# Performance work log

Hardware: AMD Instinct MI355X
Metric: run time of the kernel (lower is better)

The kernel has to match this reference:

```python
import jax, jax.numpy as jnp
import numpy as np

TAU = 0.5      # init kwarg tau
LAMBD = 0.5    # init kwarg lambd
N, D, C = 4096, 1024, 512


def setup_inputs() -> dict:
    key = jax.random.key(0)
    k1, k2, k3 = jax.random.split(key, 3)
    return {
        "layer_embeds": jax.random.normal(k1, (N, D), dtype=jnp.float32),
        "y_true": jax.random.randint(k2, (N,), 0, C),
        "y_pred": jax.random.normal(k3, (N, C), dtype=jnp.float32),
    }


def _clce(x, y_true, y_pred):
    n = x.shape[0]
    # pairwise cosine similarity via one matmul (torch eps = 1e-8)
    norms = jnp.clip(jnp.linalg.norm(x, axis=1, keepdims=True), 1e-8)
    xn = x / norms
    sim = (xn @ xn.T + 1.0) * 0.5 * TAU          # [N, N]

    same = y_true[:, None] == y_true[None, :]    # diagonal is always True
    eye = jnp.eye(n, dtype=bool)
    pos_mask = same & ~eye                        # candidate positives (j != i)
    neg_mask = ~same                              # negatives (excludes diagonal)

    # slot 0: similarity to the FIRST positive j (in j order), else stays 0
    first_pos = jnp.argmax(pos_mask, axis=1)
    has_pos = pos_mask.any(axis=1)
    slot0 = jnp.where(has_pos,
                      jnp.take_along_axis(sim, first_pos[:, None], axis=1)[:, 0],
                      0.0)

    # negatives packed left-to-right into columns 1..; unfilled slots stay 0
    cum = jnp.cumsum(neg_mask, axis=1)            # 1-based slot per negative
    cols = jnp.where(neg_mask, cum, 2 * n - 1)    # non-negatives -> sink col
    rows = jnp.arange(n)[:, None]
    loss_temp = jnp.zeros((n, 2 * n), dtype=sim.dtype)
    loss_temp = loss_temp.at[rows, cols].add(jnp.where(neg_mask, sim, 0.0))
    loss_temp = loss_temp.at[:, 0].set(slot0)
    loss_temp = loss_temp[:, : 2 * n - 1]         # drop sink column -> [N, 2N-1]

    cl = -jax.nn.log_softmax(loss_temp, axis=1)[:, 0]
    cl = cl.sum() / n

    logp = jax.nn.log_softmax(y_pred, axis=1)
    ce = -jnp.take_along_axis(logp, y_true[:, None], axis=1).mean()

    return LAMBD * cl + (1.0 - LAMBD) * ce


def reference(layer_embeds, y_true, y_pred):
    return _clce(layer_embeds, y_true, y_pred)
```

## Files before the change

kernel.cpp:

```cpp
#include <hip/hip_runtime.h>
#include <hip/hip_bf16.h>

#define NR 4096
#define DIM 1024
#define NCLS 512

typedef __attribute__((ext_vector_type(4))) float f32x4;
typedef __attribute__((ext_vector_type(8))) int v8i;

static __device__ __forceinline__ unsigned int q4(float v) {
  unsigned int s = (v < 0.f) ? 8u : 0u;
  float a = fabsf(v);
  unsigned int c;
  if (a < 0.25f) c = 0;
  else if (a < 0.75f) c = 1;
  else if (a < 1.25f) c = 2;
  else if (a < 1.75f) c = 3;
  else if (a < 2.5f) c = 4;
  else if (a < 3.5f) c = 5;
  else if (a < 5.0f) c = 6;
  else c = 7;
  return s | c;
}

__global__ __launch_bounds__(256) void k_prep(const float* __restrict__ x,
                                              const int* __restrict__ y,
                                              const float* __restrict__ yp,
                                              unsigned char* __restrict__ xnp,
                                              int* __restrict__ cnt,
                                              int* __restrict__ fpos,
                                              float* __restrict__ slot0,
                                              float* __restrict__ ce,
                                              float* __restrict__ out) {
  const int b = blockIdx.x;
  const int tid = threadIdx.x;
  if (b < 1024) {
    int row = b * 4 + (tid >> 6);
    int lane = tid & 63;
    const float4* xr = reinterpret_cast<const float4*>(x + (size_t)row * DIM);
    float4 v[4];
    float s = 0.f;
#pragma unroll
    for (int it = 0; it < 4; ++it) {
      v[it] = xr[it * 64 + lane];
      s += v[it].x * v[it].x + v[it].y * v[it].y + v[it].z * v[it].z + v[it].w * v[it].w;
    }
#pragma unroll
    for (int d = 1; d < 64; d <<= 1) s += __shfl_xor(s, d);
    float inv = 32.0f / fmaxf(sqrtf(s), 1e-8f);
    unsigned char* xo = xnp + (size_t)row * 512;
#pragma unroll
    for (int it = 0; it < 4; ++it) {
      int k0 = (it * 64 + lane) * 4;
      int pos = (k0 >> 7) * 64 + ((k0 >> 5) & 3) * 16 + ((k0 & 31) >> 1);
      unsigned int n0 = q4(v[it].x * inv), n1 = q4(v[it].y * inv),
                   n2 = q4(v[it].z * inv), n3 = q4(v[it].w * inv);
      unsigned short pk =
          (unsigned short)(n0 | (n1 << 4) | (n2 << 8) | (n3 << 12));
      *(unsigned short*)(xo + pos) = pk;
    }
  } else if (b < 2048) {
    int row = (b - 1024) * 4 + (tid >> 6);
    int lane = tid & 63;
    const float4* p = reinterpret_cast<const float4*>(yp + (size_t)row * NCLS);
    float4 v0 = p[lane], v1 = p[lane + 64];
    float m = fmaxf(fmaxf(fmaxf(v0.x, v0.y), fmaxf(v0.z, v0.w)),
                    fmaxf(fmaxf(v1.x, v1.y), fmaxf(v1.z, v1.w)));
#pragma unroll
    for (int d = 1; d < 64; d <<= 1) m = fmaxf(m, __shfl_xor(m, d));
    float s = __expf(v0.x - m) + __expf(v0.y - m) + __expf(v0.z - m) + __expf(v0.w - m) +
              __expf(v1.x - m) + __expf(v1.y - m) + __expf(v1.z - m) + __expf(v1.w - m);
#pragma unroll
    for (int d = 1; d < 64; d <<= 1) s += __shfl_xor(s, d);
    if (lane == 0) {
      float py = yp[(size_t)row * NCLS + y[row]];
      ce[row] = logf(s) + m - py;
    }
  } else {
    __shared__ int ys[NR];
    __shared__ int scnt[NCLS], sm1[NCLS], sm2[NCLS];
    for (int j = tid; j < NR; j += 256) ys[j] = y[j];
    for (int c = tid; c < NCLS; c += 256) { scnt[c] = 0; sm1[c] = NR; sm2[c] = NR; }
    __syncthreads();
    for (int i = tid; i < NR; i += 256) {
      int c = ys[i];
      atomicAdd(&scnt[c], 1);
      atomicMin(&sm1[c], i);
    }
    __syncthreads();
    for (int i = tid; i < NR; i += 256) {
      int c = ys[i];
      if (sm1[c] != i) atomicMin(&sm2[c], i);
    }
    __syncthreads();
    for (int i = tid; i < NR; i += 256) {
      int c = ys[i];
      int m1 = sm1[c];
      int j = (m1 == i) ? ((sm2[c] >= NR) ? -1 : sm2[c]) : m1;
      fpos[i] = j;
      slot0[i] = 0.f;
    }
    for (int c = tid; c < NCLS; c += 256) cnt[c] = scnt[c];
    if (tid == 0) out[0] = 0.f;
  }
}


#define STAGE(SSLOT, GROWBASE, KT)                                               \
  {                                                                              \
    const char* _src = (const char*)xnp +                                        \
        (size_t)((GROWBASE) + srow) * 512 + (size_t)(KT) * 64 + scol;            \
    __builtin_amdgcn_global_load_lds(                                            \
        (const __attribute__((address_space(1))) void*)_src,                     \
        (__attribute__((address_space(3))) void*)(lds + (SSLOT) + tid * 16),     \
        16, 0, 0);                                                               \
  }

#define PHASE(BUFB, RP, LOADB, SSLOT, SBASE, SKT, VM)                            \
  {                                                                              \
    _Pragma("unroll") for (int mm = 0; mm < 2; ++mm) {                           \
      int4 t4 = *(const int4*)(lds + (BUFB) + ABaseW +                           \
                               ((RP) * 2 + mm) * 1024);                          \
      v8i tv = {t4.x, t4.y, t4.z, t4.w, 0, 0, 0, 0};                             \
      afr[mm] = tv;                                                              \
    }                                                                            \
    if (LOADB) {                                                                 \
      _Pragma("unroll") for (int nf = 0; nf < 2; ++nf) {                         \
        int4 t4 = *(const int4*)(lds + (BUFB) + BBaseW + nf * 1024);             \
        v8i tv = {t4.x, t4.y, t4.z, t4.w, 0, 0, 0, 0};                           \
        bfr[nf] = tv;                                                            \
      }                                                                          \
    }                                                                            \
    STAGE(SSLOT, SBASE, SKT)                                                     \
    if (VM) asm volatile("s_waitcnt vmcnt(1)" ::: "memory");                     \
    __builtin_amdgcn_s_barrier();                                                \
    asm volatile("s_waitcnt lgkmcnt(0)" ::: "memory");                           \
    __builtin_amdgcn_sched_barrier(0);                                           \
    __builtin_amdgcn_s_setprio(1);                                               \
    _Pragma("unroll") for (int mm = 0; mm < 2; ++mm)                             \
      _Pragma("unroll") for (int nf = 0; nf < 2; ++nf)                           \
        acc[(RP) * 2 + mm][nf] = __builtin_amdgcn_mfma_scale_f32_16x16x128_f8f6f4( \
            afr[mm], bfr[nf], acc[(RP) * 2 + mm][nf], 4, 4,                      \
            0, 0x7F7F7F7F, 0, 0x7F7F7F7F);                                       \
    __builtin_amdgcn_s_setprio(0);                                               \
    __builtin_amdgcn_sched_barrier(0);                                           \
    __builtin_amdgcn_s_barrier();                                                \
  }

__global__ __launch_bounds__(512, 2) void k_gemm(const unsigned char* __restrict__ xnp,
                                                 const int* __restrict__ y,
                                                 const int* __restrict__ fpos,
                                                 float* __restrict__ part,
                                                 float* __restrict__ slot0) {
  __shared__ char lds[32768];
  const int tid = threadIdx.x;
  const int w = tid >> 6, lane = tid & 63;
  const int wr = w >> 2, wcn = w & 3;
  const int r0 = lane & 15, klo = lane >> 4;

  const int bid = blockIdx.x;
  const int swzb = (bid & 7) * 128 + (bid >> 3);
  const int rb = swzb >> 5, cb = swzb & 31;
  const int rowbase = rb * 128, colbase = cb * 128;

  const int kread = (klo * 16) ^ ((r0 & 3) << 4);
  const int ABaseW = wr * 4096 + r0 * 64 + kread;
  const int BBaseW = 8192 + wcn * 2048 + r0 * 64 + kread;

  int srow, scol;
  {
    int D = tid * 16;
    int L = D ^ (((D >> 6) & 3) << 4);
    srow = L >> 6;
    scol = L & 63;
  }

  f32x4 acc[4][2] = {};

  STAGE(8192, colbase, 0)
  STAGE(0, rowbase, 0)
  STAGE(24576, colbase, 1)
  asm volatile("s_waitcnt vmcnt(1)" ::: "memory");
  __builtin_amdgcn_s_barrier();

  for (int i = 0; i < 4; ++i) {
    const int t1 = 2 * i + 1;
    const int tn = (2 * i + 2 < 8) ? 2 * i + 2 : 7;
    const int tn1 = (2 * i + 3 < 8) ? 2 * i + 3 : 7;
    v8i afr[2], bfr[2];
    PHASE(0,     0, 1, 16384, rowbase, t1, 0)
    PHASE(0,     1, 0, 8192,  colbase, tn, 1)
    PHASE(16384, 0, 1, 0,     rowbase, tn, 0)
    PHASE(16384, 1, 0, 24576, colbase, tn1, 1)
  }

  asm volatile("s_waitcnt vmcnt(0)" ::: "memory");
  __syncthreads();

  int* yrow_s = (int*)lds;
  int* ycol_s = (int*)(lds + 512);
  int* frow_s = (int*)(lds + 1024);
  float* rsum = (float*)(lds + 2048);
  if (tid < 128) {
    yrow_s[tid] = y[rowbase + tid];
    frow_s[tid] = fpos[rowbase + tid];
  } else if (tid < 256) {
    ycol_s[tid - 128] = y[colbase + tid - 128];
  }
  __syncthreads();

#pragma unroll
  for (int m = 0; m < 4; ++m) {
    float rs[4] = {0.f, 0.f, 0.f, 0.f};
    int rloc[4], yr[4], fr[4];
#pragma unroll
    for (int reg = 0; reg < 4; ++reg) {
      rloc[reg] = wr * 64 + m * 16 + klo * 4 + reg;
      yr[reg] = yrow_s[rloc[reg]];
      fr[reg] = frow_s[rloc[reg]];
    }
#pragma unroll
    for (int nf = 0; nf < 2; ++nf) {
      int cl = wcn * 32 + nf * 16 + r0;
      int yc = ycol_s[cl];
      int gc = colbase + cl;
#pragma unroll
      for (int reg = 0; reg < 4; ++reg) {
        float sv = acc[m][nf][reg] * (1.0f / 4096.f) + 0.25f;
        float e = (yr[reg] == yc) ? 0.f : __expf(sv);
        rs[reg] += e;
        if (fr[reg] == gc) slot0[rowbase + rloc[reg]] = sv;
      }
    }
#pragma unroll
    for (int d = 1; d < 16; d <<= 1)
#pragma unroll
      for (int reg = 0; reg < 4; ++reg) rs[reg] += __shfl_xor(rs[reg], d);
    if (r0 == 0) {
#pragma unroll
      for (int reg = 0; reg < 4; ++reg)
        rsum[rloc[reg] * 4 + wcn] = rs[reg];
    }
  }
  __syncthreads();
  if (tid < 128)
    part[(size_t)cb * NR + rowbase + tid] =
        rsum[tid * 4] + rsum[tid * 4 + 1] + rsum[tid * 4 + 2] + rsum[tid * 4 + 3];
}

__global__ __launch_bounds__(256) void k_final(const float* __restrict__ part,
                                               const float* __restrict__ slot0,
                                               const int* __restrict__ cnt,
                                               const int* __restrict__ y,
                                               const float* __restrict__ ce,
                                               float* __restrict__ out) {
  __shared__ float red[256];
  const int tid = threadIdx.x;
  const int r = blockIdx.x * 256 + tid;
  float S = 0.f;
#pragma unroll
  for (int b = 0; b < 32; ++b) S += part[(size_t)b * NR + r];
  float s0 = slot0[r];
  float zeros = 4094.0f + (float)cnt[y[r]];
  float cl = logf(__expf(s0) + S + zeros) - s0;
  red[tid] = 0.5f * (cl + ce[r]);
  __syncthreads();
  for (int s = 128; s > 0; s >>= 1) {
    if (tid < s) red[tid] += red[tid + s];
    __syncthreads();
  }
  if (tid == 0) atomicAdd(out, red[0] / (float)NR);
}

extern "C" void kernel_launch(void* const* d_in, const int* in_sizes, int n_in,
                              void* d_out, int out_size, void* d_ws, size_t ws_size,
                              hipStream_t stream) {
  const float* x = (const float*)d_in[0];
  const int* y = (const int*)d_in[1];
  const float* yp = (const float*)d_in[2];
  float* out = (float*)d_out;

  char* w = (char*)d_ws;
  unsigned char* xnp = (unsigned char*)w;
  int* cnt = (int*)(w + 2097152);
  int* fpos = (int*)(w + 2099200);
  float* slot0 = (float*)(w + 2115584);
  float* part = (float*)(w + 2131968);
  float* ce = (float*)(w + 2656256);

  k_prep<<<2049, 256, 0, stream>>>(x, y, yp, xnp, cnt, fpos, slot0, ce, out);
  k_gemm<<<1024, 512, 0, stream>>>(xnp, y, fpos, part, slot0);
  k_final<<<16, 256, 0, stream>>>(part, slot0, cnt, y, ce, out);
}
```

Measured before the change: 48.12 us.

## Enlarge GEMM tile to 256x128 with simple double-buffered K loop

The similarity GEMM tile grows from 128x128 to 256x128 per block, with the 8 waves rearranged as 4x2 and each wave holding a 64x64 accumulator (4x4 MFMA fragments). The launch goes from 1024 to 512 blocks. The hand-pipelined phase schedule with split barriers and priority changes is replaced by a plain double buffer: stage the next K chunk, compute the current one, then sync. This increases operand reuse per LDS load and halves the block count, at the cost of more LDS (48KB), more accumulator registers, fewer blocks to fill the CUs, and coarser load/compute overlap.

```diff
diff --git a/kernel.cpp b/kernel.cpp
--- a/kernel.cpp
+++ b/kernel.cpp
@@ -106,45 +106,24 @@
 }
 
 
-#define STAGE(SSLOT, GROWBASE, KT)                                               \
+#define STAGE_CHUNK(BUFB, KT)                                                    \
   {                                                                              \
-    const char* _src = (const char*)xnp +                                        \
-        (size_t)((GROWBASE) + srow) * 512 + (size_t)(KT) * 64 + scol;            \
+    _Pragma("unroll") for (int q = 0; q < 2; ++q) {                              \
+      const char* _srcA = (const char*)xnp +                                     \
+          (size_t)(rowbase + srowA[q]) * 512 + (size_t)(KT) * 64 + scolA[q];     \
+      __builtin_amdgcn_global_load_lds(                                          \
+          (const __attribute__((address_space(1))) void*)_srcA,                  \
+          (__attribute__((address_space(3))) void*)(lds + (BUFB) + q * 8192 +    \
+                                                    tid * 16),                   \
+          16, 0, 0);                                                             \
+    }                                                                            \
+    const char* _srcB = (const char*)xnp +                                       \
+        (size_t)(colbase + srowB) * 512 + (size_t)(KT) * 64 + scolB;             \
     __builtin_amdgcn_global_load_lds(                                            \
-        (const __attribute__((address_space(1))) void*)_src,                     \
-        (__attribute__((address_space(3))) void*)(lds + (SSLOT) + tid * 16),     \
+        (const __attribute__((address_space(1))) void*)_srcB,                    \
+        (__attribute__((address_space(3))) void*)(lds + (BUFB) + 16384 +         \
+                                                  tid * 16),                     \
         16, 0, 0);                                                               \
-  }
-
-#define PHASE(BUFB, RP, LOADB, SSLOT, SBASE, SKT, VM)                            \
-  {                                                                              \
-    _Pragma("unroll") for (int mm = 0; mm < 2; ++mm) {                           \
-      int4 t4 = *(const int4*)(lds + (BUFB) + ABaseW +                           \
-                               ((RP) * 2 + mm) * 1024);                          \
-      v8i tv = {t4.x, t4.y, t4.z, t4.w, 0, 0, 0, 0};                             \
-      afr[mm] = tv;                                                              \
-    }                                                                            \
-    if (LOADB) {                                                                 \
-      _Pragma("unroll") for (int nf = 0; nf < 2; ++nf) {                         \
-        int4 t4 = *(const int4*)(lds + (BUFB) + BBaseW + nf * 1024);             \
-        v8i tv = {t4.x, t4.y, t4.z, t4.w, 0, 0, 0, 0};                           \
-        bfr[nf] = tv;                                                            \
-      }                                                                          \
-    }                                                                            \
-    STAGE(SSLOT, SBASE, SKT)                                                     \
-    if (VM) asm volatile("s_waitcnt vmcnt(1)" ::: "memory");                     \
-    __builtin_amdgcn_s_barrier();                                                \
-    asm volatile("s_waitcnt lgkmcnt(0)" ::: "memory");                           \
-    __builtin_amdgcn_sched_barrier(0);                                           \
-    __builtin_amdgcn_s_setprio(1);                                               \
-    _Pragma("unroll") for (int mm = 0; mm < 2; ++mm)                             \
-      _Pragma("unroll") for (int nf = 0; nf < 2; ++nf)                           \
-        acc[(RP) * 2 + mm][nf] = __builtin_amdgcn_mfma_scale_f32_16x16x128_f8f6f4( \
-            afr[mm], bfr[nf], acc[(RP) * 2 + mm][nf], 4, 4,                      \
-            0, 0x7F7F7F7F, 0, 0x7F7F7F7F);                                       \
-    __builtin_amdgcn_s_setprio(0);                                               \
-    __builtin_amdgcn_sched_barrier(0);                                           \
-    __builtin_amdgcn_s_barrier();                                                \
   }
 
 __global__ __launch_bounds__(512, 2) void k_gemm(const unsigned char* __restrict__ xnp,
@@ -152,81 +131,103 @@
                                                  const int* __restrict__ fpos,
                                                  float* __restrict__ part,
                                                  float* __restrict__ slot0) {
-  __shared__ char lds[32768];
+  __shared__ char lds[49152];
   const int tid = threadIdx.x;
   const int w = tid >> 6, lane = tid & 63;
-  const int wr = w >> 2, wcn = w & 3;
+  const int wr = w >> 1, wc = w & 1;
   const int r0 = lane & 15, klo = lane >> 4;
 
   const int bid = blockIdx.x;
-  const int swzb = (bid & 7) * 128 + (bid >> 3);
+  const int swzb = (bid & 7) * 64 + (bid >> 3);
   const int rb = swzb >> 5, cb = swzb & 31;
-  const int rowbase = rb * 128, colbase = cb * 128;
+  const int rowbase = rb * 256, colbase = cb * 128;
 
   const int kread = (klo * 16) ^ ((r0 & 3) << 4);
-  const int ABaseW = wr * 4096 + r0 * 64 + kread;
-  const int BBaseW = 8192 + wcn * 2048 + r0 * 64 + kread;
-
-  int srow, scol;
+  const int ABase = wr * 4096 + r0 * 64 + kread;
+  const int BBase = 16384 + wc * 4096 + r0 * 64 + kread;
+
+  int srowA[2], scolA[2], srowB, scolB;
+#pragma unroll
+  for (int q = 0; q < 2; ++q) {
+    int D = q * 8192 + tid * 16;
+    int L = D ^ (((D >> 6) & 3) << 4);
+    srowA[q] = L >> 6;
+    scolA[q] = L & 63;
+  }
   {
     int D = tid * 16;
     int L = D ^ (((D >> 6) & 3) << 4);
-    srow = L >> 6;
-    scol = L & 63;
-  }
-
-  f32x4 acc[4][2] = {};
-
-  STAGE(8192, colbase, 0)
-  STAGE(0, rowbase, 0)
-  STAGE(24576, colbase, 1)
-  asm volatile("s_waitcnt vmcnt(1)" ::: "memory");
-  __builtin_amdgcn_s_barrier();
-
-  for (int i = 0; i < 4; ++i) {
-    const int t1 = 2 * i + 1;
-    const int tn = (2 * i + 2 < 8) ? 2 * i + 2 : 7;
-    const int tn1 = (2 * i + 3 < 8) ? 2 * i + 3 : 7;
-    v8i afr[2], bfr[2];
-    PHASE(0,     0, 1, 16384, rowbase, t1, 0)
-    PHASE(0,     1, 0, 8192,  colbase, tn, 1)
-    PHASE(16384, 0, 1, 0,     rowbase, tn, 0)
-    PHASE(16384, 1, 0, 24576, colbase, tn1, 1)
-  }
-
-  asm volatile("s_waitcnt vmcnt(0)" ::: "memory");
-  __syncthreads();
+    srowB = L >> 6;
+    scolB = L & 63;
+  }
+
+  f32x4 acc[4][4] = {};
+
+  STAGE_CHUNK(0, 0)
+  __syncthreads();
+
+#pragma unroll
+  for (int t = 0; t < 8; ++t) {
+    const int bufb = (t & 1) ? 24576 : 0;
+    const int nbuf = (t & 1) ? 0 : 24576;
+    if (t < 7) STAGE_CHUNK(nbuf, t + 1)
+    v8i afr[4];
+#pragma unroll
+    for (int mm = 0; mm < 4; ++mm) {
+      int4 t4 = *(const int4*)(lds + bufb + ABase + mm * 1024);
+      v8i tv = {t4.x, t4.y, t4.z, t4.w, 0, 0, 0, 0};
+      afr[mm] = tv;
+    }
+#pragma unroll
+    for (int nh = 0; nh < 2; ++nh) {
+      v8i bfr[2];
+#pragma unroll
+      for (int nf = 0; nf < 2; ++nf) {
+        int4 t4 = *(const int4*)(lds + bufb + BBase + (nh * 2 + nf) * 1024);
+        v8i tv = {t4.x, t4.y, t4.z, t4.w, 0, 0, 0, 0};
+        bfr[nf] = tv;
+      }
+#pragma unroll
+      for (int mm = 0; mm < 4; ++mm)
+#pragma unroll
+        for (int nf = 0; nf < 2; ++nf)
+          acc[mm][nh * 2 + nf] = __builtin_amdgcn_mfma_scale_f32_16x16x128_f8f6f4(
+              afr[mm], bfr[nf], acc[mm][nh * 2 + nf], 4, 4,
+              0, 0x7F7F7F7F, 0, 0x7F7F7F7F);
+    }
+    __syncthreads();
+  }
 
   int* yrow_s = (int*)lds;
-  int* ycol_s = (int*)(lds + 512);
-  int* frow_s = (int*)(lds + 1024);
-  float* rsum = (float*)(lds + 2048);
-  if (tid < 128) {
+  int* ycol_s = (int*)(lds + 1024);
+  int* frow_s = (int*)(lds + 1536);
+  float* rsum = (float*)(lds + 2560);
+  if (tid < 256) {
     yrow_s[tid] = y[rowbase + tid];
     frow_s[tid] = fpos[rowbase + tid];
-  } else if (tid < 256) {
-    ycol_s[tid - 128] = y[colbase + tid - 128];
-  }
-  __syncthreads();
-
-#pragma unroll
-  for (int m = 0; m < 4; ++m) {
+  } else if (tid < 384) {
+    ycol_s[tid - 256] = y[colbase + tid - 256];
+  }
+  __syncthreads();
+
+#pragma unroll
+  for (int mf = 0; mf < 4; ++mf) {
     float rs[4] = {0.f, 0.f, 0.f, 0.f};
     int rloc[4], yr[4], fr[4];
 #pragma unroll
     for (int reg = 0; reg < 4; ++reg) {
-      rloc[reg] = wr * 64 + m * 16 + klo * 4 + reg;
+      rloc[reg] = wr * 64 + mf * 16 + klo * 4 + reg;
       yr[reg] = yrow_s[rloc[reg]];
       fr[reg] = frow_s[rloc[reg]];
     }
 #pragma unroll
-    for (int nf = 0; nf < 2; ++nf) {
-      int cl = wcn * 32 + nf * 16 + r0;
+    for (int nf = 0; nf < 4; ++nf) {
+      int cl = wc * 64 + nf * 16 + r0;
       int yc = ycol_s[cl];
       int gc = colbase + cl;
 #pragma unroll
       for (int reg = 0; reg < 4; ++reg) {
-        float sv = acc[m][nf][reg] * (1.0f / 4096.f) + 0.25f;
+        float sv = acc[mf][nf][reg] * (1.0f / 4096.f) + 0.25f;
         float e = (yr[reg] == yc) ? 0.f : __expf(sv);
         rs[reg] += e;
         if (fr[reg] == gc) slot0[rowbase + rloc[reg]] = sv;
@@ -239,13 +240,12 @@
     if (r0 == 0) {
 #pragma unroll
       for (int reg = 0; reg < 4; ++reg)
-        rsum[rloc[reg] * 4 + wcn] = rs[reg];
-    }
-  }
-  __syncthreads();
-  if (tid < 128)
-    part[(size_t)cb * NR + rowbase + tid] =
-        rsum[tid * 4] + rsum[tid * 4 + 1] + rsum[tid * 4 + 2] + rsum[tid * 4 + 3];
+        rsum[rloc[reg] * 2 + wc] = rs[reg];
+    }
+  }
+  __syncthreads();
+  if (tid < 256)
+    part[(size_t)cb * NR + rowbase + tid] = rsum[tid * 2] + rsum[tid * 2 + 1];
 }
 
 __global__ __launch_bounds__(256) void k_final(const float* __restrict__ part,
@@ -289,6 +289,6 @@
   float* ce = (float*)(w + 2656256);
 
   k_prep<<<2049, 256, 0, stream>>>(x, y, yp, xnp, cnt, fpos, slot0, ce, out);
-  k_gemm<<<1024, 512, 0, stream>>>(xnp, y, fpos, part, slot0);
+  k_gemm<<<512, 512, 0, stream>>>(xnp, y, fpos, part, slot0);
   k_final<<<16, 256, 0, stream>>>(part, slot0, cnt, y, ce, out);
 }
```

Result: slower. 53.81 us (+11.8%).

## Exploit symmetry of similarity matrix to compute only upper-triangular tiles

Applied to the files above, without the earlier changes.

Launches blocks only for upper-triangular 128x128 tiles of the pairwise similarity GEMM, mapping block index to (row, col) tile with a small loop. Off-diagonal tiles also reduce column-wise exp sums and write the transposed partial sums and first-positive similarities. This roughly halves the matmul work, at the cost of extra epilogue reductions and fewer blocks to fill the GPU.

```diff
diff --git a/kernel.cpp b/kernel.cpp
--- a/kernel.cpp
+++ b/kernel.cpp
@@ -159,9 +159,11 @@
   const int r0 = lane & 15, klo = lane >> 4;
 
   const int bid = blockIdx.x;
-  const int swzb = (bid & 7) * 128 + (bid >> 3);
-  const int rb = swzb >> 5, cb = swzb & 31;
+  int t = (bid & 7) * 66 + (bid >> 3), rb = 0;
+  while (t >= 32 - rb) { t -= 32 - rb; ++rb; }
+  const int cb = rb + t;
   const int rowbase = rb * 128, colbase = cb * 128;
+  const bool offd = (rb != cb);
 
   const int kread = (klo * 16) ^ ((r0 & 3) << 4);
   const int ABaseW = wr * 4096 + r0 * 64 + kread;
@@ -200,15 +202,19 @@
   int* yrow_s = (int*)lds;
   int* ycol_s = (int*)(lds + 512);
   int* frow_s = (int*)(lds + 1024);
+  int* fcol_s = (int*)(lds + 1536);
   float* rsum = (float*)(lds + 2048);
+  float* csum = (float*)(lds + 4096);
   if (tid < 128) {
     yrow_s[tid] = y[rowbase + tid];
     frow_s[tid] = fpos[rowbase + tid];
   } else if (tid < 256) {
     ycol_s[tid - 128] = y[colbase + tid - 128];
+    fcol_s[tid - 128] = fpos[colbase + tid - 128];
   }
   __syncthreads();
 
+  float csn[2] = {0.f, 0.f};
 #pragma unroll
   for (int m = 0; m < 4; ++m) {
     float rs[4] = {0.f, 0.f, 0.f, 0.f};
@@ -223,13 +229,17 @@
     for (int nf = 0; nf < 2; ++nf) {
       int cl = wcn * 32 + nf * 16 + r0;
       int yc = ycol_s[cl];
+      int fc = fcol_s[cl];
       int gc = colbase + cl;
 #pragma unroll
       for (int reg = 0; reg < 4; ++reg) {
         float sv = acc[m][nf][reg] * (1.0f / 4096.f) + 0.25f;
         float e = (yr[reg] == yc) ? 0.f : __expf(sv);
         rs[reg] += e;
-        if (fr[reg] == gc) slot0[rowbase + rloc[reg]] = sv;
+        csn[nf] += e;
+        int gr = rowbase + rloc[reg];
+        if (fr[reg] == gc) slot0[gr] = sv;
+        if (offd && fc == gr) slot0[gc] = sv;
       }
     }
 #pragma unroll
@@ -242,10 +252,23 @@
         rsum[rloc[reg] * 4 + wcn] = rs[reg];
     }
   }
+#pragma unroll
+  for (int nf = 0; nf < 2; ++nf) {
+    csn[nf] += __shfl_xor(csn[nf], 16);
+    csn[nf] += __shfl_xor(csn[nf], 32);
+  }
+  if (klo == 0) {
+#pragma unroll
+    for (int nf = 0; nf < 2; ++nf)
+      csum[(wcn * 32 + nf * 16 + r0) * 2 + wr] = csn[nf];
+  }
   __syncthreads();
-  if (tid < 128)
+  if (tid < 128) {
     part[(size_t)cb * NR + rowbase + tid] =
         rsum[tid * 4] + rsum[tid * 4 + 1] + rsum[tid * 4 + 2] + rsum[tid * 4 + 3];
+    if (offd)
+      part[(size_t)rb * NR + colbase + tid] = csum[tid * 2] + csum[tid * 2 + 1];
+  }
 }
 
 __global__ __launch_bounds__(256) void k_final(const float* __restrict__ part,
@@ -289,6 +312,6 @@
   float* ce = (float*)(w + 2656256);
 
   k_prep<<<2049, 256, 0, stream>>>(x, y, yp, xnp, cnt, fpos, slot0, ce, out);
-  k_gemm<<<1024, 512, 0, stream>>>(xnp, y, fpos, part, slot0);
+  k_gemm<<<528, 512, 0, stream>>>(xnp, y, fpos, part, slot0);
   k_final<<<16, 256, 0, stream>>>(part, slot0, cnt, y, ce, out);
 }
```

New measurement: 45.21 us. 1.06x faster.
